# Optimization experiments

Hardware: AMD Instinct MI355X
Metric: run time of the kernel (lower is better)

Reference implementation:

```python
import jax, jax.numpy as jnp
import numpy as np

B, C, H, W = 2, 256, 64, 64
FEAT = 256          # in_channels * expansion_ratio
HEADS = 8
HS = FEAT // HEADS  # 32
OUT = 256


def setup_inputs() -> dict:
    key = jax.random.key(0)
    ks = jax.random.split(key, 12)
    inp = {
        "x": jax.random.normal(ks[0], (B, C, H, W), jnp.float32),
        "mod_multiplier": jax.random.normal(ks[1], (B, FEAT), jnp.float32),
        "mod_bias": jax.random.normal(ks[2], (B, FEAT), jnp.float32),
        # learned parameters (1x1 convs as matrices)
        "w_qkv": jax.random.normal(ks[3], (3 * FEAT, C), jnp.float32) * 0.02,
        "b_qkv": jnp.zeros((3 * FEAT,), jnp.float32),
        "w_proj": jax.random.normal(ks[4], (OUT, FEAT), jnp.float32) * 0.02,
        "pe_q_h": jax.random.normal(ks[5], (1, FEAT, H, 1), jnp.float32) * 0.02,
        "pe_q_w": jax.random.normal(ks[6], (1, FEAT, 1, W), jnp.float32) * 0.02,
        "pe_k_h": jax.random.normal(ks[7], (1, FEAT, H, 1), jnp.float32) * 0.02,
        "pe_k_w": jax.random.normal(ks[8], (1, FEAT, 1, W), jnp.float32) * 0.02,
        "pre_act_bias": jnp.zeros((1, C, 1, 1), jnp.float32),
        "pre_qkv_bias": jnp.zeros((1, C, 1, 1), jnp.float32),
        "pre_proj_bias": jnp.zeros((1, FEAT, 1, 1), jnp.float32),
        "id_scale": jnp.ones((1, OUT, 1, 1), jnp.float32),
    }
    return inp


def reference(x, mod_multiplier, mod_bias, w_qkv, b_qkv, w_proj,
              pe_q_h, pe_q_w, pe_k_h, pe_k_w,
              pre_act_bias, pre_qkv_bias, pre_proj_bias, id_scale):
    b = x.shape[0]
    # pre-activation (Fixup-style biases)
    x_preact = jax.nn.silu(x + pre_act_bias) + pre_qkv_bias
    # 1x1 conv -> QKV: [b, 3F, H, W]
    qkv = jnp.einsum('bchw,oc->bohw', x_preact, w_qkv) + b_qkv[None, :, None, None]
    q, k, v = jnp.split(qkv, 3, axis=1)
    # additive positional embeddings
    q = q + pe_q_h + pe_q_w
    k = k + pe_k_h + pe_k_w
    # FiLM modulation of query
    q = q * mod_multiplier[:, :, None, None] + mod_bias[:, :, None, None]
    # [b, heads, head_size, H*W]
    q = q.reshape(b, HEADS, HS, H * W)
    k = k.reshape(b, HEADS, HS, H * W)
    v = v.reshape(b, HEADS, HS, H * W)
    scale = jnp.asarray(HS ** 0.5, x.dtype)
    logits = jnp.einsum('bhdn,bhdm->bhnm', q, k) / scale
    weights = jax.nn.softmax(logits, axis=-1)
    attn = jnp.einsum('bhnm,bhdm->bhdn', weights, v)
    attn = attn.reshape(b, FEAT, H, W)
    # output projection (1x1 conv, no bias)
    x_res = jnp.einsum('bchw,oc->bohw', attn + pre_proj_bias, w_proj)
    return x * id_scale + x_res
```

## Files before the change

kernel.cpp:

```cpp
#include <hip/hip_runtime.h>
#include <hip/hip_bf16.h>
#include <cstdint>

#define NB   2
#define NC   256
#define NN   4096
#define NH   8
#define HSZ  32
#define NF   256
#define N3F  768

typedef __bf16 bf16x8 __attribute__((ext_vector_type(8)));
typedef __bf16 bf16x4 __attribute__((ext_vector_type(4)));
typedef short  s16x4  __attribute__((ext_vector_type(4)));
typedef float  floatx4 __attribute__((ext_vector_type(4)));

#define QSCALE 0.25506601622184f

#define PIECE 2097152

#define GLD16(gsrc, ldst)                                                             \
    __builtin_amdgcn_global_load_lds(                                                 \
        (const __attribute__((address_space(1))) unsigned int*)(gsrc),                \
        (__attribute__((address_space(3))) unsigned int*)(ldst), 16, 0, 0)

__global__ void k_prep(const float* __restrict__ x, const float* __restrict__ pab,
                       const float* __restrict__ pqb, __bf16* __restrict__ y,
                       const float* __restrict__ wqkv, const float* __restrict__ wproj,
                       __bf16* __restrict__ wqb, __bf16* __restrict__ wpb) {
    __shared__ __bf16 ct[32 * 264];
    int bid = blockIdx.x, tid = threadIdx.x;
    if (bid >= 256) {
        int id = (bid - 256) * 1024 + tid * 4;
        const float* src = (id < 196608) ? (wqkv + id) : (wproj + (id - 196608));
        __bf16* dst = (id < 196608) ? (wqb + id) : (wpb + (id - 196608));
        float4 v = *(const float4*)src;
        bf16x4 o;
        o[0] = (__bf16)v.x; o[1] = (__bf16)v.y; o[2] = (__bf16)v.z; o[3] = (__bf16)v.w;
        *(bf16x4*)dst = o;
        return;
    }
    int b = bid >> 7, nt = bid & 127;
    int n0 = nt * 32;
    int cbase = tid >> 3, nc = tid & 7;
#pragma unroll
    for (int q = 0; q < 8; q++) {
        int c = cbase + q * 32;
        const float4 xv = *(const float4*)(x + ((size_t)b * NC + c) * NN + n0 + nc * 4);
        float bias = pab[c], qb = pqb[c];
        float vs[4] = {xv.x, xv.y, xv.z, xv.w};
#pragma unroll
        for (int i = 0; i < 4; i++) {
            float s = vs[i] + bias;
            float r = s / (1.f + __expf(-s)) + qb;
            ct[(nc * 4 + i) * 264 + c] = (__bf16)r;
        }
    }
    __syncthreads();
#pragma unroll
    for (int q = 0; q < 4; q++) {
        int id = tid + q * 256;
        int n = id >> 5, ck = (id & 31) * 8;
        bf16x8 v = *(const bf16x8*)(ct + n * 264 + ck);
        *(bf16x8*)(y + ((size_t)b * NN + n0 + n) * NC + ck) = v;
    }
}

__launch_bounds__(256)
__global__ void k_qkv(const __bf16* __restrict__ y, const __bf16* __restrict__ wb,
                      const float* __restrict__ bqkv,
                      const float* __restrict__ peqh, const float* __restrict__ peqw,
                      const float* __restrict__ pekh, const float* __restrict__ pekw,
                      const float* __restrict__ mm, const float* __restrict__ mb,
                      __bf16* __restrict__ qs, __bf16* __restrict__ kf, __bf16* __restrict__ vf) {
    __shared__ __bf16 smem[4][64 * 40];
    __bf16* ct = &smem[0][0];
    const int nt = blockIdx.x, ot = blockIdx.y, b = blockIdx.z;
    const int tid = threadIdx.x;
    const int wave = tid >> 6, lane = tid & 63, ln = lane & 15, quad = lane >> 4;
    const int wm = (wave & 1) * 32, wn = (wave >> 1) * 32;
    floatx4 acc[2][2];
#pragma unroll
    for (int i = 0; i < 2; i++)
#pragma unroll
        for (int j = 0; j < 2; j++) acc[i][j] = 0.f;
    const __bf16* ysrc = y + ((size_t)b * NN + nt * 64) * NC;
    const __bf16* wsrc = wb + (size_t)ot * 64 * NC;
    const int r0 = tid >> 2, c0 = (tid & 3) * 8;
    bf16x8 ya[2], wa[2];
    ya[0] = *(const bf16x8*)(ysrc + (size_t)r0 * NC + c0);
    wa[0] = *(const bf16x8*)(wsrc + (size_t)r0 * NC + c0);
#pragma unroll 2
    for (int ko = 0; ko < 8; ko++) {
        int cur = ko & 1, nxt = cur ^ 1;
        *(bf16x8*)(&smem[cur][r0 * 40 + c0]) = ya[cur];
        *(bf16x8*)(&smem[2 + cur][r0 * 40 + c0]) = wa[cur];
        if (ko < 7) {
            int kc = (ko + 1) * 32;
            ya[nxt] = *(const bf16x8*)(ysrc + (size_t)r0 * NC + kc + c0);
            wa[nxt] = *(const bf16x8*)(wsrc + (size_t)r0 * NC + kc + c0);
        }
        __syncthreads();
        bf16x8 af[2], bfr[2];
#pragma unroll
        for (int ii = 0; ii < 2; ii++) af[ii]  = *(const bf16x8*)(&smem[cur][(wm + ii * 16 + ln) * 40 + quad * 8]);
#pragma unroll
        for (int jj = 0; jj < 2; jj++) bfr[jj] = *(const bf16x8*)(&smem[2 + cur][(wn + jj * 16 + ln) * 40 + quad * 8]);
#pragma unroll
        for (int ii = 0; ii < 2; ii++)
#pragma unroll
            for (int jj = 0; jj < 2; jj++)
                acc[ii][jj] = __builtin_amdgcn_mfma_f32_16x16x32_bf16(af[ii], bfr[jj], acc[ii][jj], 0, 0, 0);
    }
    __syncthreads();
    if (ot < 8) {
#pragma unroll
        for (int ii = 0; ii < 2; ii++)
#pragma unroll
            for (int jj = 0; jj < 2; jj++) {
                int o_l = wn + jj * 16 + ln;
                int o_g = ot * 64 + o_l;
                float bq = bqkv[o_g];
#pragma unroll
                for (int r = 0; r < 4; r++) {
                    int n_l = wm + ii * 16 + quad * 4 + r;
                    float val = acc[ii][jj][r] + bq;
                    if (ot < 4) {
                        val += peqh[o_g * 64 + nt] + peqw[o_g * 64 + n_l];
                        val = val * mm[b * NF + o_g] + mb[b * NF + o_g];
                        val *= QSCALE;
                    } else {
                        int c = o_g - 256;
                        val += pekh[c * 64 + nt] + pekw[c * 64 + n_l];
                    }
                    ct[n_l * 72 + o_l] = (__bf16)val;
                }
            }
        __syncthreads();
#pragma unroll
        for (int q = 0; q < 2; q++) {
            int id = tid + q * 256;
            int n_l = id >> 3, oc = (id & 7) * 8;
            bf16x8 v = *(const bf16x8*)(ct + n_l * 72 + oc);
            int n_g = nt * 64 + n_l;
            int o_g = ot * 64 + oc;
            if (ot < 4) {
                int h = o_g >> 5, d = o_g & 31;
                *(bf16x8*)(qs + (((size_t)b * NH + h) * NN + n_g) * HSZ + d) = v;
            } else {
                int c = o_g - 256, h = c >> 5, d0 = c & 31;
                size_t blk = ((size_t)(b * NH + h) * 256 + (n_g >> 4)) * 512;
                *(bf16x8*)(kf + blk + (d0 >> 3) * 128 + (n_g & 15) * 8) = v;
            }
        }
    } else {
#pragma unroll
        for (int ii = 0; ii < 2; ii++)
#pragma unroll
            for (int jj = 0; jj < 2; jj++) {
                int o_l = wn + jj * 16 + ln;
                float bq = bqkv[ot * 64 + o_l];
#pragma unroll
                for (int r = 0; r < 4; r++) {
                    int n_l = wm + ii * 16 + quad * 4 + r;
                    ct[o_l * 72 + n_l] = (__bf16)(acc[ii][jj][r] + bq);
                }
            }
        __syncthreads();
#pragma unroll
        for (int q = 0; q < 4; q++) {
            int id = tid + q * 256;
            int o_l = id >> 4, ng4 = (id & 15) * 4;
            bf16x4 v = *(const bf16x4*)(ct + o_l * 72 + ng4);
            int c = (ot - 8) * 64 + o_l, h = c >> 5, d = c & 31;
            int dj = d >> 4, lnv = d & 15;
            int m_g = nt * 64 + ng4;
            size_t blk = ((size_t)(b * NH + h) * 256 + (m_g >> 4)) * 512;
            *(bf16x4*)(vf + blk + (((m_g >> 2) & 3) * 16 + lnv) * 8 + dj * 4) = v;
        }
    }
}

__launch_bounds__(256, 8)
__global__ void k_attn(const __bf16* __restrict__ qs, const __bf16* __restrict__ kf,
                       const __bf16* __restrict__ vf,
                       __bf16* __restrict__ po012, __bf16* __restrict__ po3,
                       float* __restrict__ pl) {
    __shared__ __bf16 sbuf[8192];
    int bi = blockIdx.x;
    int xcd = bi & 7, r = bi >> 3;
    int bh = xcd * 2 + (r & 1);
    int r2 = r >> 1;
    int qt = r2 & 31, piece = r2 >> 5;
    int tid = threadIdx.x, wave = tid >> 6, lane = tid & 63, ln = lane & 15, quad = lane >> 4;
    int n0 = qt * 128 + wave * 32;
    const __bf16* qbase = qs + (size_t)bh * NN * HSZ;
    const __bf16* kfb = kf + ((size_t)bh * 256 + piece * 64) * 512;
    const __bf16* vfb = vf + ((size_t)bh * 256 + piece * 64) * 512;
    bf16x8 qa[2];
    qa[0] = *(const bf16x8*)(qbase + (size_t)(n0 + ln) * HSZ + quad * 8);
    qa[1] = *(const bf16x8*)(qbase + (size_t)(n0 + 16 + ln) * HSZ + quad * 8);
    floatx4 o[2][2], o2[2];
    o[0][0] = 0.f; o[0][1] = 0.f; o[1][0] = 0.f; o[1][1] = 0.f;
    o2[0] = 0.f; o2[1] = 0.f;
    floatx4 zf = 0.f;
    s16x4 ones;
    ones[0] = (short)0x3F80; ones[1] = (short)0x3F80;
    ones[2] = (short)0x3F80; ones[3] = (short)0x3F80;
    const int toff = tid * 8;
    const int lo = lane * 8;
    for (int mt = 0; mt < 8; mt++) {
        const __bf16* kn = kfb + mt * 4096;
        const __bf16* vn = vfb + mt * 4096;
        GLD16(kn + toff,        sbuf + toff);
        GLD16(kn + toff + 2048, sbuf + toff + 2048);
        GLD16(vn + toff,        sbuf + 4096 + toff);
        GLD16(vn + toff + 2048, sbuf + 4096 + toff + 2048);
        __syncthreads();
        __builtin_amdgcn_s_setprio(1);
#pragma unroll
        for (int j = 0; j < 8; j++) {
            bf16x8 kfr = *(const bf16x8*)(sbuf + j * 512 + lo);
            bf16x8 vfr = *(const bf16x8*)(sbuf + 4096 + j * 512 + lo);
            s16x4 vb0, vb1;
            __builtin_memcpy(&vb0, &vfr, 8);
            __builtin_memcpy(&vb1, (const char*)&vfr + 8, 8);
#pragma unroll
            for (int i = 0; i < 2; i++) {
                floatx4 s = __builtin_amdgcn_mfma_f32_16x16x32_bf16(kfr, qa[i], zf, 0, 0, 0);
                bf16x4 p;
#pragma unroll
                for (int rr = 0; rr < 4; rr++)
                    p[rr] = (__bf16)__builtin_amdgcn_exp2f(s[rr]);
                s16x4 pa;
                __builtin_memcpy(&pa, &p, 8);
                o[i][0] = __builtin_amdgcn_mfma_f32_16x16x16bf16_1k(pa, vb0, o[i][0], 0, 0, 0);
                o[i][1] = __builtin_amdgcn_mfma_f32_16x16x16bf16_1k(pa, vb1, o[i][1], 0, 0, 0);
                o2[i]   = __builtin_amdgcn_mfma_f32_16x16x16bf16_1k(pa, ones, o2[i], 0, 0, 0);
            }
        }
        __builtin_amdgcn_s_setprio(0);
        __syncthreads();
    }
    size_t plbase = (size_t)(piece * 16 + bh) * NN;
    if (ln == 0)
#pragma unroll
        for (int i = 0; i < 2; i++)
#pragma unroll
            for (int rr = 0; rr < 4; rr++)
                pl[plbase + n0 + i * 16 + quad * 4 + rr] = o2[i][rr];
    __bf16* ct = sbuf;
#pragma unroll
    for (int i = 0; i < 2; i++)
#pragma unroll
        for (int dj = 0; dj < 2; dj++)
#pragma unroll
            for (int rr = 0; rr < 4; rr++)
                ct[(wave * 32 + i * 16 + quad * 4 + rr) * 32 + dj * 16 + ln] = (__bf16)o[i][dj][rr];
    __syncthreads();
    __bf16* pob = (piece < 3) ? (po012 + (size_t)piece * PIECE) : po3;
    size_t pobase = ((size_t)bh * NN + (size_t)qt * 128) * HSZ;
#pragma unroll
    for (int q = 0; q < 2; q++) {
        int id = tid + q * 256;
        int n_l = id >> 2, dc = (id & 3) * 8;
        *(bf16x8*)(pob + pobase + n_l * HSZ + dc) = *(const bf16x8*)(ct + n_l * 32 + dc);
    }
}

__launch_bounds__(256)
__global__ void k_proj(const __bf16* __restrict__ po012, const __bf16* __restrict__ po3,
                       const float* __restrict__ pl,
                       const __bf16* __restrict__ wpb, const float* __restrict__ ppb,
                       const float* __restrict__ x, const float* __restrict__ idsc,
                       float* __restrict__ out) {
    __shared__ __bf16 at[32 * 264];
    __shared__ __bf16 bt[2][64 * 40];
    __shared__ float linv[8 * 64];
    __shared__ float ppbs[256];
    int nt = blockIdx.x, ot = blockIdx.y, b = blockIdx.z;
    int tid = threadIdx.x, wave = tid >> 6, lane = tid & 63, ln = lane & 15, quad = lane >> 4;
    int wo = (wave & 1) * 16, wn = (wave >> 1) * 32;
#pragma unroll
    for (int q = 0; q < 4; q++) {
        int id = tid + q * 256;
        int row = id >> 5, fc = (id & 31) * 8;
        *(bf16x8*)(at + row * 264 + fc) = *(const bf16x8*)(wpb + (size_t)(ot * 32 + row) * NF + fc);
    }
#pragma unroll
    for (int q = 0; q < 2; q++) {
        int id = tid + q * 256;
        int h = id >> 6, n_l = id & 63;
        size_t base = (size_t)(b * NH + h) * NN + nt * 64 + n_l;
        linv[id] = 1.f / (pl[base] + pl[base + (size_t)16 * NN]
                        + pl[base + (size_t)32 * NN] + pl[base + (size_t)48 * NN]);
    }
    ppbs[tid] = ppb[tid];
    __syncthreads();
    floatx4 acc[2];
    acc[0] = 0.f; acc[1] = 0.f;
    const int n_l = tid >> 2, dh8 = (tid & 3) * 8;
    const size_t hstep = (size_t)NN * HSZ;
    size_t prow = ((size_t)b * NH * NN + (size_t)nt * 64 + n_l) * HSZ + dh8;
    bf16x8 p0[2], p1[2], p2[2], p3[2];
    p0[0] = *(const bf16x8*)(po012 + prow);
    p1[0] = *(const bf16x8*)(po012 + prow + (size_t)PIECE);
    p2[0] = *(const bf16x8*)(po012 + prow + (size_t)2 * PIECE);
    p3[0] = *(const bf16x8*)(po3 + prow);
#pragma unroll 2
    for (int ko = 0; ko < 8; ko++) {
        int cur = ko & 1, nxt = cur ^ 1;
        float iv = linv[ko * 64 + n_l];
        bf16x8 c;
#pragma unroll
        for (int e = 0; e < 8; e++)
            c[e] = (__bf16)(((float)p0[cur][e] + (float)p1[cur][e]
                           + (float)p2[cur][e] + (float)p3[cur][e]) * iv
                           + ppbs[ko * 32 + dh8 + e]);
        *(bf16x8*)(&bt[cur][n_l * 40 + dh8]) = c;
        if (ko < 7) {
            size_t pr = prow + (size_t)(ko + 1) * hstep;
            p0[nxt] = *(const bf16x8*)(po012 + pr);
            p1[nxt] = *(const bf16x8*)(po012 + pr + (size_t)PIECE);
            p2[nxt] = *(const bf16x8*)(po012 + pr + (size_t)2 * PIECE);
            p3[nxt] = *(const bf16x8*)(po3 + pr);
        }
        __syncthreads();
        bf16x8 af, bfr[2];
        af = *(const bf16x8*)(at + (wo + ln) * 264 + ko * 32 + quad * 8);
#pragma unroll
        for (int nj = 0; nj < 2; nj++) bfr[nj] = *(const bf16x8*)(&bt[cur][(wn + nj * 16 + ln) * 40 + quad * 8]);
#pragma unroll
        for (int nj = 0; nj < 2; nj++)
            acc[nj] = __builtin_amdgcn_mfma_f32_16x16x32_bf16(af, bfr[nj], acc[nj], 0, 0, 0);
    }
#pragma unroll
    for (int nj = 0; nj < 2; nj++)
#pragma unroll
        for (int r = 0; r < 4; r++) {
            int o_g = ot * 32 + wo + quad * 4 + r;
            int n_g = nt * 64 + wn + nj * 16 + ln;
            size_t idx = ((size_t)b * NF + o_g) * NN + n_g;
            out[idx] = x[idx] * idsc[o_g] + acc[nj][r];
        }
}

extern "C" void kernel_launch(void* const* d_in, const int* in_sizes, int n_in,
                              void* d_out, int out_size, void* d_ws, size_t ws_size,
                              hipStream_t stream) {
    (void)in_sizes; (void)n_in; (void)out_size; (void)ws_size;
    const float* x    = (const float*)d_in[0];
    const float* mm   = (const float*)d_in[1];
    const float* mb   = (const float*)d_in[2];
    const float* wqkv = (const float*)d_in[3];
    const float* bqkv = (const float*)d_in[4];
    const float* wproj= (const float*)d_in[5];
    const float* peqh = (const float*)d_in[6];
    const float* peqw = (const float*)d_in[7];
    const float* pekh = (const float*)d_in[8];
    const float* pekw = (const float*)d_in[9];
    const float* pab  = (const float*)d_in[10];
    const float* pqb  = (const float*)d_in[11];
    const float* ppb  = (const float*)d_in[12];
    const float* idsc = (const float*)d_in[13];
    float* out = (float*)d_out;

    __bf16* ws = (__bf16*)d_ws;
    const size_t SEG = 2097152;
    __bf16* y     = ws;
    __bf16* qs    = ws + SEG;
    __bf16* kf    = ws + SEG * 2;
    __bf16* vf    = ws + SEG * 3;
    __bf16* po012 = ws + SEG * 4;
    __bf16* po3   = ws;
    float*  pl    = (float*)(ws + SEG * 7);
    __bf16* wqb   = ws + SEG * 7 + 524288;
    __bf16* wpb   = wqb + 196608;

    hipLaunchKernelGGL(k_prep, dim3(512), dim3(256), 0, stream,
                       x, pab, pqb, y, wqkv, wproj, wqb, wpb);
    hipLaunchKernelGGL(k_qkv,  dim3(64, 12, 2), dim3(256), 0, stream,
                       y, wqb, bqkv, peqh, peqw, pekh, pekw, mm, mb, qs, kf, vf);
    hipLaunchKernelGGL(k_attn, dim3(2048), dim3(256), 0, stream,
                       qs, kf, vf, po012, po3, pl);
    hipLaunchKernelGGL(k_proj, dim3(64, 8, 2), dim3(256), 0, stream,
                       po012, po3, pl, wpb, ppb, x, idsc, out);
}
```

Before: 167.4 us.

## Double-buffer K/V tiles in attention kernel with async global-to-LDS prefetch

Splits the attention K/V staging into two half-size LDS buffers and prefetches the tile two steps ahead with global_load_lds, using manual vmcnt waits and raw barriers. This is meant to hide global load latency behind the MFMA/exp compute instead of stalling on every tile. The trade-off is twice as many iterations and barriers, each with half the compute. LDS footprint is unchanged. Correctness depends on the hand-written waitcnt accounting.

```diff
diff --git a/kernel.cpp b/kernel.cpp
--- a/kernel.cpp
+++ b/kernel.cpp
@@ -186,7 +186,7 @@
                        const __bf16* __restrict__ vf,
                        __bf16* __restrict__ po012, __bf16* __restrict__ po3,
                        float* __restrict__ pl) {
-    __shared__ __bf16 sbuf[8192];
+    __shared__ __bf16 sbuf[2][4096];
     int bi = blockIdx.x;
     int xcd = bi & 7, r = bi >> 3;
     int bh = xcd * 2 + (r & 1);
@@ -209,19 +209,22 @@
     ones[2] = (short)0x3F80; ones[3] = (short)0x3F80;
     const int toff = tid * 8;
     const int lo = lane * 8;
-    for (int mt = 0; mt < 8; mt++) {
-        const __bf16* kn = kfb + mt * 4096;
-        const __bf16* vn = vfb + mt * 4096;
-        GLD16(kn + toff,        sbuf + toff);
-        GLD16(kn + toff + 2048, sbuf + toff + 2048);
-        GLD16(vn + toff,        sbuf + 4096 + toff);
-        GLD16(vn + toff + 2048, sbuf + 4096 + toff + 2048);
-        __syncthreads();
+    GLD16(kfb + toff,        &sbuf[0][0] + toff);
+    GLD16(vfb + toff,        &sbuf[0][0] + 2048 + toff);
+    GLD16(kfb + 2048 + toff, &sbuf[1][0] + toff);
+    GLD16(vfb + 2048 + toff, &sbuf[1][0] + 2048 + toff);
+    for (int mt = 0; mt < 16; mt++) {
+        int cur = mt & 1;
+        const __bf16* kl = &sbuf[0][0] + cur * 4096;
+        const __bf16* vl = kl + 2048;
+        if (mt < 15) asm volatile("s_waitcnt vmcnt(2)" ::: "memory");
+        else         asm volatile("s_waitcnt vmcnt(0)" ::: "memory");
+        __builtin_amdgcn_s_barrier();
         __builtin_amdgcn_s_setprio(1);
 #pragma unroll
-        for (int j = 0; j < 8; j++) {
-            bf16x8 kfr = *(const bf16x8*)(sbuf + j * 512 + lo);
-            bf16x8 vfr = *(const bf16x8*)(sbuf + 4096 + j * 512 + lo);
+        for (int j = 0; j < 4; j++) {
+            bf16x8 kfr = *(const bf16x8*)(kl + j * 512 + lo);
+            bf16x8 vfr = *(const bf16x8*)(vl + j * 512 + lo);
             s16x4 vb0, vb1;
             __builtin_memcpy(&vb0, &vfr, 8);
             __builtin_memcpy(&vb1, (const char*)&vfr + 8, 8);
@@ -240,7 +243,14 @@
             }
         }
         __builtin_amdgcn_s_setprio(0);
-        __syncthreads();
+        asm volatile("s_waitcnt lgkmcnt(0)" ::: "memory");
+        __builtin_amdgcn_s_barrier();
+        if (mt < 14) {
+            const __bf16* kn = kfb + (size_t)(mt + 2) * 2048;
+            const __bf16* vn = vfb + (size_t)(mt + 2) * 2048;
+            GLD16(kn + toff, &sbuf[0][0] + cur * 4096 + toff);
+            GLD16(vn + toff, &sbuf[0][0] + cur * 4096 + 2048 + toff);
+        }
     }
     size_t plbase = (size_t)(piece * 16 + bh) * NN;
     if (ln == 0)
@@ -249,7 +259,7 @@
 #pragma unroll
             for (int rr = 0; rr < 4; rr++)
                 pl[plbase + n0 + i * 16 + quad * 4 + rr] = o2[i][rr];
-    __bf16* ct = sbuf;
+    __bf16* ct = &sbuf[0][0];
 #pragma unroll
     for (int i = 0; i < 2; i++)
 #pragma unroll
```

Result: no change. 168.0 us (+0.4%).
